# Kernel tuning notes

Hardware: AMD Instinct MI355X
Metric: run time of the kernel (lower is better)

Reference implementation:

```python
import jax, jax.numpy as jnp
import numpy as np

N_NODES = 100000
N_EDGES = 1600000
N_GRAPHS = 512
IN_F, H1, H2 = 128, 128, 256
N_GROUPS, N_FAM = 16, 10


def setup_inputs() -> dict:
    key = jax.random.key(0)
    ks = jax.random.split(key, 8)
    x = jax.random.normal(ks[0], (N_NODES, IN_F), dtype=jnp.float32)
    edge_index = jax.random.randint(ks[1], (2, N_EDGES), 0, N_NODES, dtype=jnp.int64)
    batch = jnp.sort(jax.random.randint(ks[2], (N_NODES,), 0, N_GRAPHS, dtype=jnp.int64))
    W1 = jax.random.normal(ks[3], (IN_F, H1), dtype=jnp.float32) / np.sqrt(IN_F)
    b1 = jnp.zeros((H1,), dtype=jnp.float32)
    W2 = jax.random.normal(ks[4], (H1, H2), dtype=jnp.float32) / np.sqrt(H1)
    b2 = jnp.zeros((H2,), dtype=jnp.float32)
    Wg = jax.random.normal(ks[5], (H2, N_GROUPS), dtype=jnp.float32) / np.sqrt(H2)
    bg = jnp.zeros((N_GROUPS,), dtype=jnp.float32)
    Wf = jax.random.normal(ks[6], (N_GROUPS, H2, N_FAM), dtype=jnp.float32) / np.sqrt(H2)
    bf = jnp.zeros((N_GROUPS, N_FAM), dtype=jnp.float32)
    return {"x": x, "edge_index": edge_index, "batch": batch,
            "W1": W1, "b1": b1, "W2": W2, "b2": b2,
            "Wg": Wg, "bg": bg, "Wf": Wf, "bf": bf}


def gcn_conv(x, W, b, src, dst, num_nodes):
    # PyG GCNConv: add self-loops, symmetric normalization, scatter-add aggregation.
    xw = x @ W  # [N, out]
    deg = jax.ops.segment_sum(jnp.ones((src.shape[0],), x.dtype), dst,
                              num_segments=num_nodes) + 1.0  # +1 self-loop
    dinv = jax.lax.rsqrt(deg)
    coef = dinv[src] * dinv[dst]            # [E]
    msg = xw[src] * coef[:, None]           # gather + scale (memory-bound)
    agg = jax.ops.segment_sum(msg, dst, num_segments=num_nodes)
    agg = agg + xw * (dinv * dinv)[:, None]  # self-loop contribution
    return agg + b


def reference(x, edge_index, batch, W1, b1, W2, b2, Wg, bg, Wf, bf):
    src, dst = edge_index[0], edge_index[1]
    h = jax.nn.relu(gcn_conv(x, W1, b1, src, dst, N_NODES))
    # dropout p=0.5 is identity in eval mode
    h = gcn_conv(h, W2, b2, src, dst, N_NODES)
    # global mean pool over graphs
    sums = jax.ops.segment_sum(h, batch, num_segments=N_GRAPHS)       # [G, H2]
    cnts = jax.ops.segment_sum(jnp.ones((N_NODES,), h.dtype), batch,
                               num_segments=N_GRAPHS)
    pooled = sums / jnp.maximum(cnts, 1.0)[:, None]
    group_logits = pooled @ Wg + bg                                   # [G, num_groups]
    family_logits = jnp.einsum('bd,gdf->gbf', pooled, Wf) + bf[:, None, :]
    return group_logits, family_logits
```

## Files before the change

kernel.cpp:

```cpp
#include <hip/hip_runtime.h>

#define NN 100000
#define NE 1600000
#define NGR 512
#define KF 128
#define H2F 256
#define NGRP 16
#define NFAM 10

#define CH 128
#define NCHUNK ((NN + CH - 1) / CH)
#define PT 6656
#define NT ((NE + PT - 1) / PT)
#define PREPB_BLKS 64
#define GBB ((NN + 255) / 256)

#define NSPLIT 8

typedef __attribute__((ext_vector_type(8))) short short8;
typedef __attribute__((ext_vector_type(4))) float floatx4;
typedef __attribute__((ext_vector_type(2))) float floatx2;

__device__ __forceinline__ unsigned short f2bf(float f) {
  unsigned u = __float_as_uint(f);
  unsigned r = (u + 0x7fff + ((u >> 16) & 1)) >> 16;
  return (unsigned short)r;
}
__device__ __forceinline__ unsigned short pk_fp8(float a, float b) {
  return (unsigned short)__builtin_amdgcn_cvt_pk_fp8_f32(a, b, 0, false);
}
__device__ __forceinline__ floatx2 unpk_fp8(unsigned short u) {
  return __builtin_amdgcn_cvt_pk_f32_fp8((int)u, false);
}


__global__ __launch_bounds__(256) void k_histprep(const int* __restrict__ ei,
                                                  const int* __restrict__ batch,
                                                  int* __restrict__ tot,
                                                  int* __restrict__ gb,
                                                  const float* __restrict__ W,
                                                  unsigned short* __restrict__ Bp) {
  __shared__ int lh[NCHUNK];
  int tid = threadIdx.x;
  if (blockIdx.x >= NT + PREPB_BLKS) {
    int n = (blockIdx.x - NT - PREPB_BLKS) * 256 + tid;
    if (n >= NN) return;
    int b0 = batch[n];
    if (n == 0) {
      for (int g = 0; g <= b0; ++g) gb[g] = 0;
    }
    int b1 = (n + 1 < NN) ? batch[n + 1] : NGR;
    for (int g = b0 + 1; g <= b1; ++g) gb[g] = n + 1;
    return;
  }
  if (blockIdx.x >= NT) {
    int idx = (blockIdx.x - NT) * 256 + tid;
    int j = idx & 7;
    int l = (idx >> 3) & 63;
    int rest = idx >> 9;
    int nc = rest & 7;
    int kc = rest >> 3;
    int k = kc * 32 + (l >> 4) * 8 + j;
    int nn = nc * 16 + (l & 15);
    Bp[idx] = f2bf(W[k * KF + nn]);
    return;
  }
  for (int g = tid; g < NCHUNK; g += 256) lh[g] = 0;
  __syncthreads();
  int base = blockIdx.x * PT;
  int nv = min(PT, NE - base);
  for (int i = tid; i < nv; i += 256) atomicAdd(&lh[ei[NE + base + i] >> 7], 1);
  __syncthreads();
  for (int g = tid; g < NCHUNK; g += 256) {
    int v = lh[g];
    if (v) atomicAdd(&tot[g], v);
  }
}


__global__ __launch_bounds__(256) void k_scantot(const int* __restrict__ tot,
                                                 int* __restrict__ cbase,
                                                 int* __restrict__ cursor) {
  __shared__ int ssc[256];
  int tid = threadIdx.x;
  int v4[4]; int loc = 0;
#pragma unroll
  for (int j = 0; j < 4; ++j) {
    int idx = tid * 4 + j;
    v4[j] = (idx < NCHUNK) ? tot[idx] : 0;
    loc += v4[j];
  }
  ssc[tid] = loc;
  __syncthreads();
  for (int off = 1; off < 256; off <<= 1) {
    int val = (tid >= off) ? ssc[tid - off] : 0;
    __syncthreads();
    ssc[tid] += val;
    __syncthreads();
  }
  int excl = ssc[tid] - loc;
#pragma unroll
  for (int j = 0; j < 4; ++j) {
    int idx = tid * 4 + j;
    if (idx < NCHUNK) { cbase[idx] = excl; cursor[idx] = excl; }
    excl += v4[j];
  }
  if (tid == 255) cbase[NCHUNK] = excl;
}


__global__ __launch_bounds__(256) void k_pscatter(const int* __restrict__ ei,
                                                  int* __restrict__ cursor,
                                                  int2* __restrict__ erec) {
  __shared__ int2 stage[PT];
  __shared__ int lstart[NCHUNK];
  __shared__ int lrun[NCHUNK];
  __shared__ int gbase[NCHUNK];
  __shared__ int ssc[256];
  int t0 = blockIdx.x, tid = threadIdx.x;
  for (int g = tid; g < NCHUNK; g += 256) lrun[g] = 0;
  __syncthreads();
  int base = t0 * PT;
  int nv = min(PT, NE - base);
  for (int i = tid; i < nv; i += 256) atomicAdd(&lrun[ei[NE + base + i] >> 7], 1);
  __syncthreads();
  int v4[4]; int loc = 0;
#pragma unroll
  for (int j = 0; j < 4; ++j) {
    int idx = tid * 4 + j;
    v4[j] = (idx < NCHUNK) ? lrun[idx] : 0;
    loc += v4[j];
  }
  ssc[tid] = loc;
  __syncthreads();
  for (int off = 1; off < 256; off <<= 1) {
    int val = (tid >= off) ? ssc[tid - off] : 0;
    __syncthreads();
    ssc[tid] += val;
    __syncthreads();
  }
  int excl = ssc[tid] - loc;
#pragma unroll
  for (int j = 0; j < 4; ++j) {
    int idx = tid * 4 + j;
    if (idx < NCHUNK) lstart[idx] = excl;
    excl += v4[j];
  }
  __syncthreads();
  for (int g = tid; g < NCHUNK; g += 256) {
    int cnt = ((g + 1 < NCHUNK) ? lstart[g + 1] : nv) - lstart[g];
    gbase[g] = cnt ? atomicAdd(&cursor[g], cnt) : 0;
    lrun[g] = lstart[g];
  }
  __syncthreads();
  for (int i = tid; i < nv; i += 256) {
    int s = ei[base + i], d = ei[NE + base + i];
    int pos = atomicAdd(&lrun[d >> 7], 1);
    stage[pos] = make_int2(s, d);
  }
  __syncthreads();
  for (int j = tid; j < nv; j += 256) {
    int2 r = stage[j];
    int g = r.y >> 7;
    erec[gbase[g] + (j - lstart[g])] = r;
  }
}


__global__ __launch_bounds__(256) void k_sort(const int2* __restrict__ erec,
                                              const int* __restrict__ cbase,
                                              int* __restrict__ esrc,
                                              int* __restrict__ rowptr,
                                              float* __restrict__ dinv) {
  __shared__ int hist[CH];
  __shared__ int lrun[CH];
  __shared__ int sc[256];
  const int c = blockIdx.x, tid = threadIdx.x;
  const int e0 = cbase[c], e1 = cbase[c + 1];
  const int nv = e1 - e0;
  if (tid < CH) hist[tid] = 0;
  __syncthreads();
  for (int i = tid; i < nv; i += 256) atomicAdd(&hist[erec[e0 + i].y & (CH - 1)], 1);
  __syncthreads();
  int deg = (tid < CH) ? hist[tid] : 0;
  sc[tid] = deg;
  __syncthreads();
  for (int off = 1; off < 256; off <<= 1) {
    int val = (tid >= off) ? sc[tid - off] : 0;
    __syncthreads();
    sc[tid] += val;
    __syncthreads();
  }
  int excl = sc[tid] - deg;
  int node = c * CH + tid;
  if (tid < CH) {
    lrun[tid] = excl;
    if (node < NN) {
      rowptr[node] = e0 + excl;
      dinv[node] = rsqrtf((float)(deg + 1));
    } else if (node == NN) {
      rowptr[NN] = e0 + excl;
    }
  }
  __syncthreads();
  for (int i = tid; i < nv; i += 256) {
    int2 r = erec[e0 + i];
    int pos = atomicAdd(&lrun[r.y & (CH - 1)], 1);
    esrc[e0 + pos] = r.x;
  }
}


__global__ __launch_bounds__(256) void k_gemm_mfma(const float* __restrict__ A,
                                                   const unsigned short* __restrict__ Bp,
                                                   const float* __restrict__ dinv,
                                                   unsigned short* __restrict__ C) {
  constexpr int K = 128;
  constexpr int NCH = KF / 16;
  const int wv = blockIdx.x * 4 + (threadIdx.x >> 6);
  const int row0 = wv * 16;
  if (row0 >= NN) return;
  const int lane = threadIdx.x & 63;
  const int m = lane & 15;
  const int q = lane >> 4;

  floatx4 acc[NCH];
#pragma unroll
  for (int i = 0; i < NCH; ++i) acc[i] = (floatx4){0.f, 0.f, 0.f, 0.f};

  const int arow = row0 + m;
#pragma unroll
  for (int kc = 0; kc < 4; ++kc) {
    const float* ap = A + (size_t)arow * K + kc * 32 + q * 8;
    float4 f0 = *(const float4*)ap;
    float4 f1 = *(const float4*)(ap + 4);
    short8 af;
    af[0] = (short)f2bf(f0.x); af[1] = (short)f2bf(f0.y);
    af[2] = (short)f2bf(f0.z); af[3] = (short)f2bf(f0.w);
    af[4] = (short)f2bf(f1.x); af[5] = (short)f2bf(f1.y);
    af[6] = (short)f2bf(f1.z); af[7] = (short)f2bf(f1.w);
    const unsigned short* bp = Bp + (size_t)kc * NCH * 512;
#pragma unroll
    for (int nc = 0; nc < NCH; ++nc) {
      short8 bfr = *(const short8*)(bp + (size_t)nc * 512 + lane * 8);
      acc[nc] = __builtin_amdgcn_mfma_f32_16x16x32_bf16(af, bfr, acc[nc], 0, 0, 0);
    }
  }

  float ds[4];
#pragma unroll
  for (int r = 0; r < 4; ++r) ds[r] = dinv[row0 + q * 4 + r];
#pragma unroll
  for (int nc = 0; nc < 4; ++nc) {
#pragma unroll
    for (int r = 0; r < 4; ++r) {
      int row = row0 + q * 4 + r;
      C[(size_t)row * 64 + nc * 16 + m] =
          pk_fp8(acc[nc][r] * ds[r], acc[nc + 4][r] * ds[r]);
    }
  }
}


__global__ __launch_bounds__(128) void k_agg1(const unsigned short* __restrict__ p,
                                              const float* __restrict__ bias,
                                              const int* __restrict__ rowptr,
                                              const int* __restrict__ esrc,
                                              const float* __restrict__ dinv,
                                              unsigned short* __restrict__ outp) {
  const int n = blockIdx.x * 2 + (threadIdx.x >> 6);
  const int t = threadIdx.x & 63;
  const int u = t & 31;
  const int half = t >> 5;
  const unsigned* __restrict__ prow = (const unsigned*)p;

  float a0 = 0.f, a1 = 0.f, a2 = 0.f, a3 = 0.f;

  if (half == 0) {
    unsigned v = prow[((unsigned)n << 5) + u];
    floatx2 lo = unpk_fp8((unsigned short)(v & 0xffffu));
    floatx2 hi = unpk_fp8((unsigned short)(v >> 16));
    a0 = lo.x; a1 = lo.y; a2 = hi.x; a3 = hi.y;
  }

  const int r0 = rowptr[n];
  const int r1 = rowptr[n + 1];
  int i = r0;

#define PAIR_TIER(NP)                                                  \
  for (; i + 2 * (NP) <= r1; i += 2 * (NP)) {                          \
    const int ib = i + half;                                           \
    unsigned s[NP];                                                    \
    _Pragma("unroll") for (int j = 0; j < (NP); ++j)                   \
        s[j] = (unsigned)esrc[ib + 2 * j];                             \
    unsigned v[NP];                                                    \
    _Pragma("unroll") for (int j = 0; j < (NP); ++j)                   \
        v[j] = prow[(s[j] << 5) + u];                                  \
    _Pragma("unroll") for (int j = 0; j < (NP); ++j) {                 \
      floatx2 lo = unpk_fp8((unsigned short)(v[j] & 0xffffu));         \
      floatx2 hi = unpk_fp8((unsigned short)(v[j] >> 16));             \
      a0 += lo.x; a1 += lo.y; a2 += hi.x; a3 += hi.y;                  \
    }                                                                  \
  }

  PAIR_TIER(8)
  PAIR_TIER(4)
  PAIR_TIER(2)
  PAIR_TIER(1)
#undef PAIR_TIER

  if (i < r1 && half == 0) {
    unsigned s = (unsigned)esrc[i];
    unsigned v = prow[(s << 5) + u];
    floatx2 lo = unpk_fp8((unsigned short)(v & 0xffffu));
    floatx2 hi = unpk_fp8((unsigned short)(v >> 16));
    a0 += lo.x; a1 += lo.y; a2 += hi.x; a3 += hi.y;
  }

  a0 += __shfl_down(a0, 32, 64);
  a1 += __shfl_down(a1, 32, 64);
  a2 += __shfl_down(a2, 32, 64);
  a3 += __shfl_down(a3, 32, 64);

  if (half == 0) {
    const float dn = dinv[n];
    float2 blo = *(const float2*)(bias + 2 * u);
    float2 bhi = *(const float2*)(bias + 64 + 2 * u);
    float x0 = fmaxf(fmaf(dn, a0, blo.x), 0.f) * dn;
    float x1 = fmaxf(fmaf(dn, a1, bhi.x), 0.f) * dn;
    float x2 = fmaxf(fmaf(dn, a2, blo.y), 0.f) * dn;
    float x3 = fmaxf(fmaf(dn, a3, bhi.y), 0.f) * dn;
    unsigned lo = pk_fp8(x0, x1);
    unsigned hi = pk_fp8(x2, x3);
    ((unsigned*)outp)[((unsigned)n << 5) + u] = lo | (hi << 16);
  }
}


__global__ __launch_bounds__(256) void k_aggpart(const unsigned short* __restrict__ p,
                                                 const int* __restrict__ gb,
                                                 const int* __restrict__ rowptr,
                                                 const int* __restrict__ esrc,
                                                 const float* __restrict__ dinv,
                                                 float* __restrict__ pooled) {
  __shared__ float sacc[4][128];
  const int g = blockIdx.x / NSPLIT;
  const int part = blockIdx.x % NSPLIT;
  const int tid = threadIdx.x;
  const int start = gb[g], end = gb[g + 1];
  const int wv = tid >> 6, t = tid & 63, u = t & 31, half = t >> 5;
  const unsigned* __restrict__ prow = (const unsigned*)p;

  float a0 = 0.f, a1 = 0.f, a2 = 0.f, a3 = 0.f;

  const int nlen = end - start;
  const int nper = (nlen + NSPLIT - 1) / NSPLIT;
  const int ns = min(start + part * nper, end);
  const int ne = min(ns + nper, end);

  for (int n = ns + wv; n < ne; n += 4) {
    float t0, t1, t2, t3;
    if (half == 0) {
      unsigned v = prow[((unsigned)n << 5) + u];
      floatx2 lo = unpk_fp8((unsigned short)(v & 0xffffu));
      floatx2 hi = unpk_fp8((unsigned short)(v >> 16));
      t0 = lo.x; t1 = lo.y; t2 = hi.x; t3 = hi.y;
    } else {
      t0 = 0.f; t1 = 0.f; t2 = 0.f; t3 = 0.f;
    }
    const int r0 = rowptr[n];
    const int r1 = rowptr[n + 1];
    int i = r0;

#define PAIR_TIER(NP)                                                  \
    for (; i + 2 * (NP) <= r1; i += 2 * (NP)) {                        \
      const int ib = i + half;                                         \
      unsigned s[NP];                                                  \
      _Pragma("unroll") for (int j = 0; j < (NP); ++j)                 \
          s[j] = (unsigned)esrc[ib + 2 * j];                           \
      unsigned v[NP];                                                  \
      _Pragma("unroll") for (int j = 0; j < (NP); ++j)                 \
          v[j] = prow[(s[j] << 5) + u];                                \
      _Pragma("unroll") for (int j = 0; j < (NP); ++j) {               \
        floatx2 lo = unpk_fp8((unsigned short)(v[j] & 0xffffu));       \
        floatx2 hi = unpk_fp8((unsigned short)(v[j] >> 16));           \
        t0 += lo.x; t1 += lo.y; t2 += hi.x; t3 += hi.y;                \
      }                                                                \
    }

    PAIR_TIER(8)
    PAIR_TIER(4)
    PAIR_TIER(2)
    PAIR_TIER(1)
#undef PAIR_TIER

    if (i < r1 && half == 0) {
      unsigned s = (unsigned)esrc[i];
      unsigned v = prow[(s << 5) + u];
      floatx2 lo = unpk_fp8((unsigned short)(v & 0xffffu));
      floatx2 hi = unpk_fp8((unsigned short)(v >> 16));
      t0 += lo.x; t1 += lo.y; t2 += hi.x; t3 += hi.y;
    }

    const float dn = dinv[n];
    a0 = fmaf(dn, t0, a0); a1 = fmaf(dn, t1, a1);
    a2 = fmaf(dn, t2, a2); a3 = fmaf(dn, t3, a3);
  }

  a0 += __shfl_down(a0, 32, 64);
  a1 += __shfl_down(a1, 32, 64);
  a2 += __shfl_down(a2, 32, 64);
  a3 += __shfl_down(a3, 32, 64);
  if (half == 0) {
    sacc[wv][2 * u] = a0;
    sacc[wv][2 * u + 1] = a2;
    sacc[wv][2 * u + 64] = a1;
    sacc[wv][2 * u + 65] = a3;
  }
  __syncthreads();
  if (tid < KF) {
    float v = sacc[0][tid] + sacc[1][tid] + sacc[2][tid] + sacc[3][tid];
    atomicAdd(&pooled[(size_t)g * KF + tid], v);
  }
}


__global__ __launch_bounds__(256) void k_heads(const float* __restrict__ pooled,
                                               const int* __restrict__ gb,
                                               const float* __restrict__ W2,
                                               const float* __restrict__ b2,
                                               const float* __restrict__ Wg,
                                               const float* __restrict__ bg,
                                               const float* __restrict__ Wf,
                                               const float* __restrict__ bfb,
                                               float* __restrict__ out) {
  __shared__ float pr[KF];
  __shared__ float pp[H2F];
  const int g = blockIdx.x;
  const int tid = threadIdx.x;
  if (tid < KF) {
    float c = fmaxf((float)(gb[g + 1] - gb[g]), 1.f);
    pr[tid] = pooled[(size_t)g * KF + tid] / c;
  }
  __syncthreads();
  float acc = b2[tid];
#pragma unroll 8
  for (int d = 0; d < KF; ++d) acc = fmaf(pr[d], W2[d * H2F + tid], acc);
  pp[tid] = acc;
  __syncthreads();
  if (tid < NGRP) {
    float a = bg[tid];
    for (int d = 0; d < H2F; ++d) a = fmaf(pp[d], Wg[d * NGRP + tid], a);
    out[g * NGRP + tid] = a;
  } else if (tid >= 64 && tid < 64 + NGRP * NFAM) {
    int uu = tid - 64;
    int gg = uu / NFAM;
    int ff = uu % NFAM;
    float a = bfb[gg * NFAM + ff];
    for (int d = 0; d < H2F; ++d) a = fmaf(pp[d], Wf[(gg * H2F + d) * NFAM + ff], a);
    out[NGR * NGRP + (size_t)gg * NGR * NFAM + g * NFAM + ff] = a;
  }
}


extern "C" void kernel_launch(void* const* d_in, const int* in_sizes, int n_in,
                              void* d_out, int out_size, void* d_ws, size_t ws_size,
                              hipStream_t stream) {
  const float* x    = (const float*)d_in[0];
  const int*   ei   = (const int*)d_in[1];
  const int*   batch= (const int*)d_in[2];
  const float* W1   = (const float*)d_in[3];
  const float* b1   = (const float*)d_in[4];
  const float* W2   = (const float*)d_in[5];
  const float* b2   = (const float*)d_in[6];
  const float* Wg   = (const float*)d_in[7];
  const float* bg   = (const float*)d_in[8];
  const float* Wf   = (const float*)d_in[9];
  const float* bfb  = (const float*)d_in[10];
  float* out = (float*)d_out;

  char* w = (char*)d_ws;
  auto take = [&](size_t bytes) {
    char* p = w;
    w += (bytes + 255) & ~(size_t)255;
    return (void*)p;
  };
  int*   tot   = (int*)take((size_t)NCHUNK * 4);
  float* pooled= (float*)take((size_t)NGR * KF * 4);
  int*   gb    = (int*)take((size_t)(NGR + 1) * 4);
  int*   cbase = (int*)take((size_t)(NCHUNK + 1) * 4);
  int*   cursor= (int*)take((size_t)NCHUNK * 4);
  int2*  erec  = (int2*)take((size_t)NE * 8);
  int*   esrc  = (int*)take((size_t)NE * 4);
  int*   rowptr= (int*)take((size_t)(NN + 1) * 4);
  float* dinv  = (float*)take((size_t)NN * 4);
  unsigned short* Bp1 = (unsigned short*)take((size_t)KF * KF * 2);
  unsigned short* xw1 = (unsigned short*)take((size_t)NN * 64 * 2);
  unsigned short* h1  = (unsigned short*)take((size_t)NN * 64 * 2);

  size_t zbytes = (size_t)((char*)pooled - (char*)tot) + (size_t)NGR * KF * 4;
  hipMemsetAsync(tot, 0, zbytes, stream);

  k_histprep<<<NT + PREPB_BLKS + GBB, 256, 0, stream>>>(ei, batch, tot, gb, W1, Bp1);
  k_scantot<<<1, 256, 0, stream>>>(tot, cbase, cursor);
  k_pscatter<<<NT, 256, 0, stream>>>(ei, cursor, erec);
  k_sort<<<NCHUNK, 256, 0, stream>>>(erec, cbase, esrc, rowptr, dinv);

  k_gemm_mfma<<<1563, 256, 0, stream>>>(x, Bp1, dinv, xw1);

  k_agg1<<<NN / 2, 128, 0, stream>>>(xw1, b1, rowptr, esrc, dinv, h1);
  k_aggpart<<<NGR * NSPLIT, 256, 0, stream>>>(h1, gb, rowptr, esrc, dinv, pooled);
  k_heads<<<NGR, 256, 0, stream>>>(pooled, gb, W2, b2, Wg, bg, Wf, bfb, out);
}
```

Measured before the change: 292.6 us.

## Slice feature layout into 4 column slabs for cache-friendly gather aggregation

Measured after the change: 581.8 us. 98.8% more time.

```diff
diff --git a/kernel.cpp b/kernel.cpp
--- a/kernel.cpp
+++ b/kernel.cpp
@@ -15,7 +15,7 @@
 #define PREPB_BLKS 64
 #define GBB ((NN + 255) / 256)
 
-#define NSPLIT 8
+#define NSL 4
 
 typedef __attribute__((ext_vector_type(8))) short short8;
 typedef __attribute__((ext_vector_type(4))) float floatx4;
@@ -255,12 +255,27 @@
 #pragma unroll
     for (int r = 0; r < 4; ++r) {
       int row = row0 + q * 4 + r;
-      C[(size_t)row * 64 + nc * 16 + m] =
+      C[((size_t)nc * NN + row) * 16 + m] =
           pk_fp8(acc[nc][r] * ds[r], acc[nc + 4][r] * ds[r]);
     }
   }
 }
 
+
+#define SLICE_TIER(NJ)                                                 \
+  for (; i + 8 * (NJ) <= r1; i += 8 * (NJ)) {                          \
+    unsigned ss[NJ];                                                   \
+    _Pragma("unroll") for (int j = 0; j < (NJ); ++j)                   \
+        ss[j] = (unsigned)esrc[i + e + 8 * j];                         \
+    unsigned vv[NJ];                                                   \
+    _Pragma("unroll") for (int j = 0; j < (NJ); ++j)                   \
+        vv[j] = pslice[(ss[j] << 3) + d];                              \
+    _Pragma("unroll") for (int j = 0; j < (NJ); ++j) {                 \
+      floatx2 lo = unpk_fp8((unsigned short)(vv[j] & 0xffffu));        \
+      floatx2 hi = unpk_fp8((unsigned short)(vv[j] >> 16));            \
+      a0 += lo.x; a1 += lo.y; a2 += hi.x; a3 += hi.y;                  \
+    }                                                                  \
+  }
 
 __global__ __launch_bounds__(128) void k_agg1(const unsigned short* __restrict__ p,
                                               const float* __restrict__ bias,
@@ -268,16 +283,18 @@
                                               const int* __restrict__ esrc,
                                               const float* __restrict__ dinv,
                                               unsigned short* __restrict__ outp) {
-  const int n = blockIdx.x * 2 + (threadIdx.x >> 6);
-  const int t = threadIdx.x & 63;
-  const int u = t & 31;
-  const int half = t >> 5;
-  const unsigned* __restrict__ prow = (const unsigned*)p;
+  const int bid = blockIdx.x;
+  const int rr = bid & 7;
+  const int s = rr >> 1;
+  const int n = (bid >> 3) * 4 + (rr & 1) * 2 + (threadIdx.x >> 6);
+  const int lane = threadIdx.x & 63;
+  const int e = lane >> 3;
+  const int d = lane & 7;
+  const unsigned* __restrict__ pslice = (const unsigned*)p + (size_t)s * NN * 8;
 
   float a0 = 0.f, a1 = 0.f, a2 = 0.f, a3 = 0.f;
-
-  if (half == 0) {
-    unsigned v = prow[((unsigned)n << 5) + u];
+  if (e == 0) {
+    unsigned v = pslice[((unsigned)n << 3) + d];
     floatx2 lo = unpk_fp8((unsigned short)(v & 0xffffu));
     floatx2 hi = unpk_fp8((unsigned short)(v >> 16));
     a0 = lo.x; a1 = lo.y; a2 = hi.x; a3 = hi.y;
@@ -286,143 +303,98 @@
   const int r0 = rowptr[n];
   const int r1 = rowptr[n + 1];
   int i = r0;
-
-#define PAIR_TIER(NP)                                                  \
-  for (; i + 2 * (NP) <= r1; i += 2 * (NP)) {                          \
-    const int ib = i + half;                                           \
-    unsigned s[NP];                                                    \
-    _Pragma("unroll") for (int j = 0; j < (NP); ++j)                   \
-        s[j] = (unsigned)esrc[ib + 2 * j];                             \
-    unsigned v[NP];                                                    \
-    _Pragma("unroll") for (int j = 0; j < (NP); ++j)                   \
-        v[j] = prow[(s[j] << 5) + u];                                  \
-    _Pragma("unroll") for (int j = 0; j < (NP); ++j) {                 \
-      floatx2 lo = unpk_fp8((unsigned short)(v[j] & 0xffffu));         \
-      floatx2 hi = unpk_fp8((unsigned short)(v[j] >> 16));             \
-      a0 += lo.x; a1 += lo.y; a2 += hi.x; a3 += hi.y;                  \
-    }                                                                  \
-  }
-
-  PAIR_TIER(8)
-  PAIR_TIER(4)
-  PAIR_TIER(2)
-  PAIR_TIER(1)
-#undef PAIR_TIER
-
-  if (i < r1 && half == 0) {
-    unsigned s = (unsigned)esrc[i];
-    unsigned v = prow[(s << 5) + u];
-    floatx2 lo = unpk_fp8((unsigned short)(v & 0xffffu));
-    floatx2 hi = unpk_fp8((unsigned short)(v >> 16));
+  SLICE_TIER(8)
+  SLICE_TIER(4)
+  SLICE_TIER(2)
+  SLICE_TIER(1)
+  if (i + e < r1) {
+    unsigned ss = (unsigned)esrc[i + e];
+    unsigned vv = pslice[(ss << 3) + d];
+    floatx2 lo = unpk_fp8((unsigned short)(vv & 0xffffu));
+    floatx2 hi = unpk_fp8((unsigned short)(vv >> 16));
     a0 += lo.x; a1 += lo.y; a2 += hi.x; a3 += hi.y;
   }
 
-  a0 += __shfl_down(a0, 32, 64);
-  a1 += __shfl_down(a1, 32, 64);
-  a2 += __shfl_down(a2, 32, 64);
-  a3 += __shfl_down(a3, 32, 64);
-
-  if (half == 0) {
+  a0 += __shfl_xor(a0, 8, 64);  a1 += __shfl_xor(a1, 8, 64);
+  a2 += __shfl_xor(a2, 8, 64);  a3 += __shfl_xor(a3, 8, 64);
+  a0 += __shfl_xor(a0, 16, 64); a1 += __shfl_xor(a1, 16, 64);
+  a2 += __shfl_xor(a2, 16, 64); a3 += __shfl_xor(a3, 16, 64);
+  a0 += __shfl_xor(a0, 32, 64); a1 += __shfl_xor(a1, 32, 64);
+  a2 += __shfl_xor(a2, 32, 64); a3 += __shfl_xor(a3, 32, 64);
+
+  if (e == 0) {
     const float dn = dinv[n];
-    float2 blo = *(const float2*)(bias + 2 * u);
-    float2 bhi = *(const float2*)(bias + 64 + 2 * u);
+    const int tb = s * 16 + 2 * d;
+    float2 blo = *(const float2*)(bias + tb);
+    float2 bhi = *(const float2*)(bias + tb + 64);
     float x0 = fmaxf(fmaf(dn, a0, blo.x), 0.f) * dn;
     float x1 = fmaxf(fmaf(dn, a1, bhi.x), 0.f) * dn;
     float x2 = fmaxf(fmaf(dn, a2, blo.y), 0.f) * dn;
     float x3 = fmaxf(fmaf(dn, a3, bhi.y), 0.f) * dn;
     unsigned lo = pk_fp8(x0, x1);
     unsigned hi = pk_fp8(x2, x3);
-    ((unsigned*)outp)[((unsigned)n << 5) + u] = lo | (hi << 16);
-  }
-}
-
-
-__global__ __launch_bounds__(256) void k_aggpart(const unsigned short* __restrict__ p,
-                                                 const int* __restrict__ gb,
+    ((unsigned*)outp)[(size_t)s * NN * 8 + ((unsigned)n << 3) + d] = lo | (hi << 16);
+  }
+}
+
+__global__ __launch_bounds__(128) void k_aggpool(const unsigned short* __restrict__ p,
+                                                 const int* __restrict__ batch,
                                                  const int* __restrict__ rowptr,
                                                  const int* __restrict__ esrc,
                                                  const float* __restrict__ dinv,
                                                  float* __restrict__ pooled) {
-  __shared__ float sacc[4][128];
-  const int g = blockIdx.x / NSPLIT;
-  const int part = blockIdx.x % NSPLIT;
-  const int tid = threadIdx.x;
-  const int start = gb[g], end = gb[g + 1];
-  const int wv = tid >> 6, t = tid & 63, u = t & 31, half = t >> 5;
-  const unsigned* __restrict__ prow = (const unsigned*)p;
+  const int bid = blockIdx.x;
+  const int rr = bid & 7;
+  const int s = rr >> 1;
+  const int n = (bid >> 3) * 4 + (rr & 1) * 2 + (threadIdx.x >> 6);
+  const int lane = threadIdx.x & 63;
+  const int e = lane >> 3;
+  const int d = lane & 7;
+  const unsigned* __restrict__ pslice = (const unsigned*)p + (size_t)s * NN * 8;
 
   float a0 = 0.f, a1 = 0.f, a2 = 0.f, a3 = 0.f;
-
-  const int nlen = end - start;
-  const int nper = (nlen + NSPLIT - 1) / NSPLIT;
-  const int ns = min(start + part * nper, end);
-  const int ne = min(ns + nper, end);
-
-  for (int n = ns + wv; n < ne; n += 4) {
-    float t0, t1, t2, t3;
-    if (half == 0) {
-      unsigned v = prow[((unsigned)n << 5) + u];
-      floatx2 lo = unpk_fp8((unsigned short)(v & 0xffffu));
-      floatx2 hi = unpk_fp8((unsigned short)(v >> 16));
-      t0 = lo.x; t1 = lo.y; t2 = hi.x; t3 = hi.y;
-    } else {
-      t0 = 0.f; t1 = 0.f; t2 = 0.f; t3 = 0.f;
-    }
-    const int r0 = rowptr[n];
-    const int r1 = rowptr[n + 1];
-    int i = r0;
-
-#define PAIR_TIER(NP)                                                  \
-    for (; i + 2 * (NP) <= r1; i += 2 * (NP)) {                        \
-      const int ib = i + half;                                         \
-      unsigned s[NP];                                                  \
-      _Pragma("unroll") for (int j = 0; j < (NP); ++j)                 \
-          s[j] = (unsigned)esrc[ib + 2 * j];                           \
-      unsigned v[NP];                                                  \
-      _Pragma("unroll") for (int j = 0; j < (NP); ++j)                 \
-          v[j] = prow[(s[j] << 5) + u];                                \
-      _Pragma("unroll") for (int j = 0; j < (NP); ++j) {               \
-        floatx2 lo = unpk_fp8((unsigned short)(v[j] & 0xffffu));       \
-        floatx2 hi = unpk_fp8((unsigned short)(v[j] >> 16));           \
-        t0 += lo.x; t1 += lo.y; t2 += hi.x; t3 += hi.y;                \
-      }                                                                \
-    }
-
-    PAIR_TIER(8)
-    PAIR_TIER(4)
-    PAIR_TIER(2)
-    PAIR_TIER(1)
-#undef PAIR_TIER
-
-    if (i < r1 && half == 0) {
-      unsigned s = (unsigned)esrc[i];
-      unsigned v = prow[(s << 5) + u];
-      floatx2 lo = unpk_fp8((unsigned short)(v & 0xffffu));
-      floatx2 hi = unpk_fp8((unsigned short)(v >> 16));
-      t0 += lo.x; t1 += lo.y; t2 += hi.x; t3 += hi.y;
-    }
-
+  if (e == 0) {
+    unsigned v = pslice[((unsigned)n << 3) + d];
+    floatx2 lo = unpk_fp8((unsigned short)(v & 0xffffu));
+    floatx2 hi = unpk_fp8((unsigned short)(v >> 16));
+    a0 = lo.x; a1 = lo.y; a2 = hi.x; a3 = hi.y;
+  }
+
+  const int r0 = rowptr[n];
+  const int r1 = rowptr[n + 1];
+  int i = r0;
+  SLICE_TIER(8)
+  SLICE_TIER(4)
+  SLICE_TIER(2)
+  SLICE_TIER(1)
+  if (i + e < r1) {
+    unsigned ss = (unsigned)esrc[i + e];
+    unsigned vv = pslice[(ss << 3) + d];
+    floatx2 lo = unpk_fp8((unsigned short)(vv & 0xffffu));
+    floatx2 hi = unpk_fp8((unsigned short)(vv >> 16));
+    a0 += lo.x; a1 += lo.y; a2 += hi.x; a3 += hi.y;
+  }
+
+  a0 += __shfl_xor(a0, 8, 64);  a1 += __shfl_xor(a1, 8, 64);
+  a2 += __shfl_xor(a2, 8, 64);  a3 += __shfl_xor(a3, 8, 64);
+  a0 += __shfl_xor(a0, 16, 64); a1 += __shfl_xor(a1, 16, 64);
+  a2 += __shfl_xor(a2, 16, 64); a3 += __shfl_xor(a3, 16, 64);
+  a0 += __shfl_xor(a0, 32, 64); a1 += __shfl_xor(a1, 32, 64);
+  a2 += __shfl_xor(a2, 32, 64); a3 += __shfl_xor(a3, 32, 64);
+
+  if (e == 0) {
     const float dn = dinv[n];
-    a0 = fmaf(dn, t0, a0); a1 = fmaf(dn, t1, a1);
-    a2 = fmaf(dn, t2, a2); a3 = fmaf(dn, t3, a3);
-  }
-
-  a0 += __shfl_down(a0, 32, 64);
-  a1 += __shfl_down(a1, 32, 64);
-  a2 += __shfl_down(a2, 32, 64);
-  a3 += __shfl_down(a3, 32, 64);
-  if (half == 0) {
-    sacc[wv][2 * u] = a0;
-    sacc[wv][2 * u + 1] = a2;
-    sacc[wv][2 * u + 64] = a1;
-    sacc[wv][2 * u + 65] = a3;
-  }
-  __syncthreads();
-  if (tid < KF) {
-    float v = sacc[0][tid] + sacc[1][tid] + sacc[2][tid] + sacc[3][tid];
-    atomicAdd(&pooled[(size_t)g * KF + tid], v);
-  }
-}
+    const int g = batch[n];
+    const int tb = s * 16 + 2 * d;
+    float* base = pooled + (size_t)g * KF;
+    atomicAdd(base + tb,      dn * a0);
+    atomicAdd(base + tb + 64, dn * a1);
+    atomicAdd(base + tb + 1,  dn * a2);
+    atomicAdd(base + tb + 65, dn * a3);
+  }
+}
+
+#undef SLICE_TIER
 
 
 __global__ __launch_bounds__(256) void k_heads(const float* __restrict__ pooled,
@@ -508,7 +480,7 @@
 
   k_gemm_mfma<<<1563, 256, 0, stream>>>(x, Bp1, dinv, xw1);
 
-  k_agg1<<<NN / 2, 128, 0, stream>>>(xw1, b1, rowptr, esrc, dinv, h1);
-  k_aggpart<<<NGR * NSPLIT, 256, 0, stream>>>(h1, gb, rowptr, esrc, dinv, pooled);
+  k_agg1<<<(NN / 4) * 8, 128, 0, stream>>>(xw1, b1, rowptr, esrc, dinv, h1);
+  k_aggpool<<<(NN / 4) * 8, 128, 0, stream>>>(h1, batch, rowptr, esrc, dinv, pooled);
   k_heads<<<NGR, 256, 0, stream>>>(pooled, gb, W2, b2, Wg, bg, Wf, bfb, out);
 }
```
